# Performance work log

Measured on AMD Instinct MI355X. Metric: run time of the kernel, lower is better.

The kernel has to match this reference:

```python
import jax, jax.numpy as jnp
import numpy as np
import math

H = 1024
B, S = 4, 2048

def setup_inputs() -> dict:
    key = jax.random.key(0)
    k0, k1, k2, k3, k4 = jax.random.split(key, 5)
    scale = 1.0 / math.sqrt(H)
    return {
        "input_seq_rep": jax.random.normal(k0, (B, S, H), dtype=jnp.float32),
        "Wk": jax.random.uniform(k1, (H, H), dtype=jnp.float32, minval=-scale, maxval=scale),
        "bk": jax.random.uniform(k2, (H,), dtype=jnp.float32, minval=-scale, maxval=scale),
        "Wq": jax.random.uniform(k3, (H, H), dtype=jnp.float32, minval=-scale, maxval=scale),
        "bq": jax.random.uniform(k4, (H,), dtype=jnp.float32, minval=-scale, maxval=scale),
        "k_mul": 64,
    }

def reference(input_seq_rep, Wk, bk, Wq, bq, k_mul):
    b, s, h = input_seq_rep.shape
    x = jax.nn.relu(input_seq_rep)
    # torch Linear: x @ W.T + b
    k = jnp.einsum('bsh,oh->bso', x, Wk) + bk   # key (also used as value)
    q = jnp.einsum('bsh,oh->bso', x, Wq) + bq
    scores = jnp.einsum('bqh,bkh->bqk', q, k) / jnp.sqrt(jnp.float32(h))
    # Faithful mask: banded window only for batch index 0; other batches all-zero mask
    i = jnp.arange(s)[:, None]
    j = jnp.arange(s)[None, :]
    band = ((j <= i) & (j >= i - k_mul)).astype(jnp.float32)  # (S,S)
    mask = jnp.zeros((b, s, s), dtype=jnp.float32).at[0].set(band)
    scores = jnp.where(mask == 0, jnp.float32(-1e9), scores)
    p_attn = jax.nn.softmax(scores, axis=-1)
    out = jnp.einsum('bqk,bkh->bqh', p_attn, k)
    return out, p_attn
```

## Files before the change

kernel.cpp:

```cpp
#include <hip/hip_runtime.h>

#define SD 2048
#define HD 1024
#define BD 4

typedef __bf16 bf16_t;
typedef bf16_t bf16x8 __attribute__((ext_vector_type(8)));
typedef float f32x4 __attribute__((ext_vector_type(4)));
typedef unsigned short ushortx8 __attribute__((ext_vector_type(8)));
typedef unsigned short ushort_t;

__device__ inline unsigned short f2bf(float f) {
  return __builtin_bit_cast(unsigned short, (__bf16)f);
}

__device__ inline float bf2f(unsigned short u) {
  return __builtin_bit_cast(float, (unsigned)u << 16);
}

__device__ inline void gload_lds16(const void* g, void* l) {
  __builtin_amdgcn_global_load_lds(
      (const __attribute__((address_space(1))) void*)g,
      (__attribute__((address_space(3))) void*)l, 16, 0, 0);
}

template <int ROWS>
__device__ inline void stage_rows(const ushort_t* __restrict__ src, int r0, int k0,
                                  int tid, ushort_t* lds)
{
#pragma unroll
  for (int it = 0; it < ROWS / 32; ++it) {
    int c   = it * 256 + tid;
    int row = c >> 3;
    int kc8 = c & 7;
    int kcs = kc8 ^ (row & 7);
    gload_lds16(&src[(size_t)(r0 + row) * HD + k0 + kcs * 8], &lds[c * 8]);
  }
}

__device__ inline bf16x8 lds_frag(const ushort_t* l, int row, int kc8) {
  int kcs = kc8 ^ (row & 7);
  return *(const bf16x8*)&l[row * 64 + kcs * 8];
}

__global__ __launch_bounds__(256) void prep(
    const float* __restrict__ X, const float* __restrict__ Wk,
    const float* __restrict__ Wq, ushort_t* __restrict__ Xb,
    ushort_t* __restrict__ Wkb, ushort_t* __restrict__ Wqb)
{
  const int n8x = SD * HD / 8;
  const int n8w = HD * HD / 8;
  const int e = blockIdx.x * 256 + threadIdx.x;
  const float4* s4; ushortx8* d8; int idx; bool relu;
  if (e < n8x)            { s4 = (const float4*)X;  d8 = (ushortx8*)Xb;  idx = e;             relu = true; }
  else if (e < n8x + n8w) { s4 = (const float4*)Wk; d8 = (ushortx8*)Wkb; idx = e - n8x;       relu = false; }
  else                    { s4 = (const float4*)Wq; d8 = (ushortx8*)Wqb; idx = e - n8x - n8w; relu = false; }
  float4 a = s4[idx * 2], b4 = s4[idx * 2 + 1];
  float v[8] = {a.x, a.y, a.z, a.w, b4.x, b4.y, b4.z, b4.w};
  ushortx8 o;
#pragma unroll
  for (int j = 0; j < 8; ++j) {
    float f = v[j];
    if (relu) f = fmaxf(f, 0.0f);
    o[j] = f2bf(f);
  }
  d8[idx] = o;
}

__global__ __launch_bounds__(256, 2) void gemm_kq(
    const ushort_t* __restrict__ Xb, const ushort_t* __restrict__ Wkb,
    const ushort_t* __restrict__ Wqb, const float* __restrict__ bk,
    const float* __restrict__ bq, ushort_t* __restrict__ Kb,
    ushort_t* __restrict__ Qb, const float* __restrict__ X,
    float* __restrict__ part, float* __restrict__ patRest)
{
  __shared__ __align__(16) ushort_t lA[2][8192];
  __shared__ __align__(16) ushort_t lB[2][8192];

  const int bid = blockIdx.x;
  const int tid = threadIdx.x;

  if (bid >= 352) {
    const int f = bid - 352;
    const int nf4 = 3 * SD * (SD / 4);
    const float uf = 1.0f / SD;
    float4 v = make_float4(uf, uf, uf, uf);
    float4* p4 = (float4*)patRest;
    for (int e = f * 256 + tid; e < nf4; e += 384 * 256) p4[e] = v;
    return;
  }
  if (bid >= 256) {
    const int cid = bid - 256;
    const int b = cid >> 5;
    const int sub = cid & 31;
    const float4* Xp = (const float4*)(X + (size_t)(b + 1) * SD * HD + (size_t)sub * 64 * HD);
    float4 acc = make_float4(0.f, 0.f, 0.f, 0.f);
#pragma unroll 4
    for (int rr = 0; rr < 64; ++rr) {
      float4 v = Xp[rr * 256 + tid];
      acc.x += fmaxf(v.x, 0.f); acc.y += fmaxf(v.y, 0.f);
      acc.z += fmaxf(v.z, 0.f); acc.w += fmaxf(v.w, 0.f);
    }
    ((float4*)part)[((size_t)b * 32 + sub) * 256 + tid] = acc;
    return;
  }

  const int wg = ((bid & 7) << 5) | (bid >> 3);
  const int bm = wg >> 4, bn = wg & 15;
  const int half = bn >> 3;
  const ushort_t* Bm = half ? Wqb : Wkb;
  const int m0 = bm * 128, n0 = (bn & 7) * 128;

  const int lane = tid & 63;
  const int wave = tid >> 6;
  const int wm = wave >> 1, wn = wave & 1;

  f32x4 acc[4][4] = {};

  stage_rows<128>(Xb, m0, 0, tid, lA[0]);
  stage_rows<128>(Bm, n0, 0, tid, lB[0]);
  __syncthreads();

  for (int t = 0; t < 16; ++t) {
    const int cur = t & 1;
    if (t < 15) {
      stage_rows<128>(Xb, m0, (t + 1) * 64, tid, lA[cur ^ 1]);
      stage_rows<128>(Bm, n0, (t + 1) * 64, tid, lB[cur ^ 1]);
    }
#pragma unroll
    for (int h = 0; h < 2; ++h) {
      bf16x8 af[4], bfr[4];
#pragma unroll
      for (int mi = 0; mi < 4; ++mi)
        af[mi] = lds_frag(lA[cur], wm * 64 + mi * 16 + (lane & 15), h * 4 + (lane >> 4));
#pragma unroll
      for (int ni = 0; ni < 4; ++ni)
        bfr[ni] = lds_frag(lB[cur], wn * 64 + ni * 16 + (lane & 15), h * 4 + (lane >> 4));
#pragma unroll
      for (int mi = 0; mi < 4; ++mi)
#pragma unroll
        for (int ni = 0; ni < 4; ++ni)
          acc[mi][ni] = __builtin_amdgcn_mfma_f32_16x16x32_bf16(af[mi], bfr[ni], acc[mi][ni], 0, 0, 0);
    }
    __syncthreads();
  }

  const int rb = (lane >> 4) * 4;
  const int cc = lane & 15;
  const float* bias = half ? bq : bk;
  ushort_t* dst = half ? Qb : Kb;
#pragma unroll
  for (int ni = 0; ni < 4; ++ni) {
    int col = n0 + wn * 64 + ni * 16 + cc;
    float bv = bias[col];
#pragma unroll
    for (int mi = 0; mi < 4; ++mi) {
#pragma unroll
      for (int j = 0; j < 4; ++j) {
        int row = m0 + wm * 64 + mi * 16 + rb + j;
        dst[(size_t)row * HD + col] = f2bf(acc[mi][ni][j] + bv);
      }
    }
  }
}

__global__ __launch_bounds__(256, 2) void band_cm(
    const ushort_t* __restrict__ Q, const ushort_t* __restrict__ K,
    float* __restrict__ Sb0, float* __restrict__ Sb1,
    const float* __restrict__ part, const float* __restrict__ Wk,
    const float* __restrict__ bk, float* __restrict__ cm)
{
  __shared__ __align__(16) char smem[32768];
  const int bid = blockIdx.x;
  const int tid = threadIdx.x;

  if (bid < 126) {
    const int tt = bid >> 1;
    const int ks = bid & 1;
    const int blk = (tt + 1) >> 1;
    const int tcol = (tt + 1) & 1;
    const int m0 = blk * 64;
    const int n0 = (blk - 1 + tcol) * 64;
    float* Sb = ks ? Sb1 : Sb0;

    const int lane = tid & 63;
    const int wave = tid >> 6;
    const int wm = wave >> 1, wn = wave & 1;

    ushort_t* lA = (ushort_t*)smem;
    ushort_t* lB = (ushort_t*)(smem + 16384);

    f32x4 acc[2][2] = {};

    const int kbase = ks * 512;
    stage_rows<64>(Q, m0, kbase, tid, lA);
    stage_rows<64>(K, n0, kbase, tid, lB);
    __syncthreads();

    for (int t = 0; t < 8; ++t) {
      const int cur = t & 1;
      if (t < 7) {
        stage_rows<64>(Q, m0, kbase + (t + 1) * 64, tid, lA + (cur ^ 1) * 4096);
        stage_rows<64>(K, n0, kbase + (t + 1) * 64, tid, lB + (cur ^ 1) * 4096);
      }
#pragma unroll
      for (int h = 0; h < 2; ++h) {
        bf16x8 af[2], bfr[2];
#pragma unroll
        for (int mi = 0; mi < 2; ++mi)
          af[mi] = lds_frag(lA + cur * 4096, wm * 32 + mi * 16 + (lane & 15), h * 4 + (lane >> 4));
#pragma unroll
        for (int ni = 0; ni < 2; ++ni)
          bfr[ni] = lds_frag(lB + cur * 4096, wn * 32 + ni * 16 + (lane & 15), h * 4 + (lane >> 4));
#pragma unroll
        for (int mi = 0; mi < 2; ++mi)
#pragma unroll
          for (int ni = 0; ni < 2; ++ni)
            acc[mi][ni] = __builtin_amdgcn_mfma_f32_16x16x32_bf16(af[mi], bfr[ni], acc[mi][ni], 0, 0, 0);
      }
      __syncthreads();
    }

    const int rb = (lane >> 4) * 4;
    const int cc = lane & 15;
#pragma unroll
    for (int ni = 0; ni < 2; ++ni) {
      int ccol = tcol * 64 + wn * 32 + ni * 16 + cc;
#pragma unroll
      for (int mi = 0; mi < 2; ++mi)
#pragma unroll
        for (int j = 0; j < 4; ++j) {
          int row = m0 + wm * 32 + mi * 16 + rb + j;
          Sb[(size_t)row * 128 + ccol] = acc[mi][ni][j] * 0.03125f;
        }
    }
    return;
  }

  {
    const int cid = bid - 126;
    const int b = cid >> 4, og = cid & 15;
    float* xs = (float*)smem;
#pragma unroll
    for (int k = 0; k < 4; ++k) {
      int h = tid + 256 * k;
      float a = 0;
#pragma unroll 8
      for (int rc = 0; rc < 32; ++rc) a += part[((size_t)b * 32 + rc) * HD + h];
      xs[h] = a;
    }
    __syncthreads();
    const int o = og * 64 + (tid >> 2);
    const int q = tid & 3;
    const f32x4* wr = (const f32x4*)(Wk + (size_t)o * HD);
    const f32x4* x4 = (const f32x4*)xs;
    float a = 0;
#pragma unroll 8
    for (int i = 0; i < 64; ++i) {
      f32x4 w = wr[q * 64 + i], x = x4[q * 64 + i];
      a += w[0] * x[0] + w[1] * x[1] + w[2] * x[2] + w[3] * x[3];
    }
    a += __shfl_xor(a, 1);
    a += __shfl_xor(a, 2);
    if (q == 0) cm[b * HD + o] = a * (1.0f / SD) + bk[o];
  }
}

__global__ __launch_bounds__(256, 2) void pv_epi(
    const float* __restrict__ Sb0, const float* __restrict__ Sb1,
    const ushort_t* __restrict__ Kb, const float* __restrict__ cm,
    float* __restrict__ out0, float* __restrict__ P0,
    float* __restrict__ out123)
{
  __shared__ __align__(16) float smem[15488];
  const int bid = blockIdx.x;
  const int t = threadIdx.x;

  if (bid < 512) {
    float* Ks  = smem;
    float* spl = smem + 12288;
    const int i0 = (bid >> 3) * 32;
    const int hc = bid & 7;

    for (int e = t; e < 96 * 16; e += 256) {
      int lr = e >> 4, c8 = e & 15;
      int gr = i0 - 64 + lr;
      if (gr < 0) gr = 0;
      ushortx8 u = *(const ushortx8*)&Kb[(size_t)gr * HD + hc * 128 + c8 * 8];
      f32x4 f0 = {bf2f(u[0]), bf2f(u[1]), bf2f(u[2]), bf2f(u[3])};
      f32x4 f1 = {bf2f(u[4]), bf2f(u[5]), bf2f(u[6]), bf2f(u[7])};
      *(f32x4*)&Ks[lr * 128 + c8 * 8]     = f0;
      *(f32x4*)&Ks[lr * 128 + c8 * 8 + 4] = f1;
    }

    {
      const int r = t >> 3, sub = t & 7;
      const int i = i0 + r;
      const int jlo = (i >= 64) ? i - 64 : 0;
      const int scoff = i0 & 32;
      float sv[12];
      float m = -1e30f;
#pragma unroll
      for (int k = 0; k < 12; ++k) {
        int lj = sub + 8 * k;
        int gj = i0 - 64 + lj;
        bool val = (gj >= jlo) && (gj <= i);
        float s = -1e30f;
        if (val) {
          size_t sidx = (size_t)i * 128 + lj + scoff;
          s = Sb0[sidx] + Sb1[sidx];
        }
        sv[k] = s;
        m = fmaxf(m, s);
      }
#pragma unroll
      for (int off = 1; off < 8; off <<= 1) m = fmaxf(m, __shfl_xor(m, off));
      float p[12], sum = 0;
#pragma unroll
      for (int k = 0; k < 12; ++k) {
        p[k] = (sv[k] > -1e29f) ? __expf(sv[k] - m) : 0.0f;
        sum += p[k];
      }
#pragma unroll
      for (int off = 1; off < 8; off <<= 1) sum += __shfl_xor(sum, off);
      float inv = 1.0f / sum;
#pragma unroll
      for (int k = 0; k < 12; ++k) spl[r * 100 + sub + 8 * k] = p[k] * inv;
    }
    __syncthreads();

    const int r = t >> 3;
    const int g = t & 7;
    f32x4 a0 = {0,0,0,0}, a1 = {0,0,0,0}, a2 = {0,0,0,0}, a3 = {0,0,0,0};
    for (int lj = 0; lj < 96; ++lj) {
      float pv = spl[r * 100 + lj];
      const float* kr = &Ks[lj * 128 + g * 4];
      a0 += pv * *(const f32x4*)(kr);
      a1 += pv * *(const f32x4*)(kr + 32);
      a2 += pv * *(const f32x4*)(kr + 64);
      a3 += pv * *(const f32x4*)(kr + 96);
    }
    float* ob = out0 + (size_t)(i0 + r) * HD + hc * 128 + g * 4;
    *(f32x4*)(ob)      = a0;
    *(f32x4*)(ob + 32) = a1;
    *(f32x4*)(ob + 64) = a2;
    *(f32x4*)(ob + 96) = a3;
    return;
  }

  if (bid < 1024) {
    float* probs = smem;
    const int widx = t >> 6;
    const int lane = t & 63;
    const int i = (bid - 512) * 4 + widx;
    const int jlo = (i >= 64) ? i - 64 : 0;
    const int cnt = i - jlo + 1;
    const int base = ((i >> 6) - 1) * 64;

    float s0 = -1e30f;
    if (lane < cnt) {
      size_t c = (size_t)i * 128 + (jlo - base + lane);
      s0 = Sb0[c] + Sb1[c];
    }
    float s1 = -1e30f;
    if (cnt == 65) {
      size_t c = (size_t)i * 128 + (jlo - base + 64);
      s1 = Sb0[c] + Sb1[c];
    }
    float m = s0;
#pragma unroll
    for (int off = 1; off < 64; off <<= 1) m = fmaxf(m, __shfl_xor(m, off));
    m = fmaxf(m, s1);
    float p0 = (lane < cnt) ? __expf(s0 - m) : 0.0f;
    float p1 = (cnt == 65) ? __expf(s1 - m) : 0.0f;
    float sum = p0;
#pragma unroll
    for (int off = 1; off < 64; off <<= 1) sum += __shfl_xor(sum, off);
    sum += p1;
    float inv = 1.0f / sum;
    if (lane < cnt) probs[widx * 68 + lane] = p0 * inv;
    if (lane == 0 && cnt == 65) probs[widx * 68 + 64] = p1 * inv;
    __syncthreads();

    float4* rowp = (float4*)(P0 + (size_t)i * SD);
#pragma unroll
    for (int k = 0; k < 8; ++k) {
      int f4i = k * 64 + lane;
      int j0 = f4i * 4;
      float4 v = make_float4(0.f, 0.f, 0.f, 0.f);
      if (j0 + 3 >= jlo && j0 <= i) {
        float* vv = (float*)&v;
#pragma unroll
        for (int q = 0; q < 4; ++q) {
          int j = j0 + q;
          if (j >= jlo && j <= i) vv[q] = probs[widx * 68 + (j - jlo)];
        }
      }
      rowp[f4i] = v;
    }
    return;
  }

  {
    const int nf4 = 3 * SD * (HD / 4);
    const int per_b = SD * (HD / 4);
    const f32x4* cm4 = (const f32x4*)cm;
    f32x4* o4 = (f32x4*)out123;
    for (int idx = (bid - 1024) * 256 + t; idx < nf4; idx += 512 * 256) {
      int b = idx / per_b;
      int h4 = idx & (HD / 4 - 1);
      o4[idx] = cm4[b * (HD / 4) + h4];
    }
  }
}

extern "C" void kernel_launch(void* const* d_in, const int* in_sizes, int n_in,
                              void* d_out, int out_size, void* d_ws, size_t ws_size,
                              hipStream_t stream)
{
  (void)in_sizes; (void)n_in; (void)out_size; (void)ws_size;
  const float* X  = (const float*)d_in[0];
  const float* Wk = (const float*)d_in[1];
  const float* bk = (const float*)d_in[2];
  const float* Wq = (const float*)d_in[3];
  const float* bq = (const float*)d_in[4];

  float* out = (float*)d_out;
  float* pat = out + (size_t)BD * SD * HD;

  char* w = (char*)d_ws;
  ushort_t* Xb   = (ushort_t*)w; w += (size_t)SD * HD * 2;
  ushort_t* Wkb  = (ushort_t*)w; w += (size_t)HD * HD * 2;
  ushort_t* Wqb  = (ushort_t*)w; w += (size_t)HD * HD * 2;
  ushort_t* Kb0  = (ushort_t*)w; w += (size_t)SD * HD * 2;
  ushort_t* Q0b  = (ushort_t*)w; w += (size_t)SD * HD * 2;
  float*    part = (float*)w;    w += (size_t)3 * 32 * HD * 4;
  float*    cm   = (float*)w;    w += (size_t)3 * HD * 4;
  float*    Sb0  = (float*)w;    w += (size_t)SD * 128 * 4;
  float*    Sb1  = (float*)w;    w += (size_t)SD * 128 * 4;

  prep<<<2048, 256, 0, stream>>>(X, Wk, Wq, Xb, Wkb, Wqb);
  gemm_kq<<<736, 256, 0, stream>>>(Xb, Wkb, Wqb, bk, bq, Kb0, Q0b, X, part,
                                   pat + (size_t)SD * SD);
  band_cm<<<174, 256, 0, stream>>>(Q0b, Kb0, Sb0, Sb1, part, Wk, bk, cm);
  pv_epi<<<1536, 256, 0, stream>>>(Sb0, Sb1, Kb0, cm, out, pat, out + (size_t)SD * HD);
}
```

Baseline: 69.94 us.

## Fuse fp32-to-bf16 conversion into GEMM staging and move broadcast into band_cm

Removes the separate prep kernel: the projection GEMM now loads fp32 X and weights into registers, applies ReLU, converts them to bf16 and writes them swizzled into LDS, with the loads for the next tile issued ahead of the MFMA work. The broadcast of the per-batch column means into outputs for batches 1-3 moves from pv_epi into band_cm, which drops the cm buffer and 512 blocks from pv_epi. This removes one launch and the bf16 round trip through global memory. In exchange the GEMM reads twice the bytes per tile, holds more registers, and loses the async global-to-LDS path. band_cm's 48 mean blocks now also write the large broadcast region.

After: 75.76 us. 1.08x slower.

```diff
diff --git a/kernel.cpp b/kernel.cpp
--- a/kernel.cpp
+++ b/kernel.cpp
@@ -43,36 +43,47 @@
   return *(const bf16x8*)&l[row * 64 + kcs * 8];
 }
 
-__global__ __launch_bounds__(256) void prep(
+__device__ inline void stage_load(const float* __restrict__ src, int r0, int k0,
+                                  int tid, f32x4* regs)
+{
+#pragma unroll
+  for (int it = 0; it < 4; ++it) {
+    int c   = it * 256 + tid;
+    int row = c >> 3;
+    int kc8 = c & 7;
+    const float* g = &src[(size_t)(r0 + row) * HD + k0 + kc8 * 8];
+    regs[it * 2]     = *(const f32x4*)g;
+    regs[it * 2 + 1] = *(const f32x4*)(g + 4);
+  }
+}
+
+template <bool RELU>
+__device__ inline void stage_write(const f32x4* regs, int tid, ushort_t* lds)
+{
+#pragma unroll
+  for (int it = 0; it < 4; ++it) {
+    int c   = it * 256 + tid;
+    int row = c >> 3;
+    int kc8 = c & 7;
+    int kcs = kc8 ^ (row & 7);
+    f32x4 v0 = regs[it * 2], v1 = regs[it * 2 + 1];
+    ushortx8 o;
+#pragma unroll
+    for (int j = 0; j < 4; ++j) {
+      float f0 = v0[j], f1 = v1[j];
+      if (RELU) { f0 = fmaxf(f0, 0.f); f1 = fmaxf(f1, 0.f); }
+      o[j] = f2bf(f0); o[4 + j] = f2bf(f1);
+    }
+    *(ushortx8*)&lds[row * 64 + kcs * 8] = o;
+  }
+}
+
+__global__ __launch_bounds__(256, 2) void gemm_kq(
     const float* __restrict__ X, const float* __restrict__ Wk,
-    const float* __restrict__ Wq, ushort_t* __restrict__ Xb,
-    ushort_t* __restrict__ Wkb, ushort_t* __restrict__ Wqb)
-{
-  const int n8x = SD * HD / 8;
-  const int n8w = HD * HD / 8;
-  const int e = blockIdx.x * 256 + threadIdx.x;
-  const float4* s4; ushortx8* d8; int idx; bool relu;
-  if (e < n8x)            { s4 = (const float4*)X;  d8 = (ushortx8*)Xb;  idx = e;             relu = true; }
-  else if (e < n8x + n8w) { s4 = (const float4*)Wk; d8 = (ushortx8*)Wkb; idx = e - n8x;       relu = false; }
-  else                    { s4 = (const float4*)Wq; d8 = (ushortx8*)Wqb; idx = e - n8x - n8w; relu = false; }
-  float4 a = s4[idx * 2], b4 = s4[idx * 2 + 1];
-  float v[8] = {a.x, a.y, a.z, a.w, b4.x, b4.y, b4.z, b4.w};
-  ushortx8 o;
-#pragma unroll
-  for (int j = 0; j < 8; ++j) {
-    float f = v[j];
-    if (relu) f = fmaxf(f, 0.0f);
-    o[j] = f2bf(f);
-  }
-  d8[idx] = o;
-}
-
-__global__ __launch_bounds__(256, 2) void gemm_kq(
-    const ushort_t* __restrict__ Xb, const ushort_t* __restrict__ Wkb,
-    const ushort_t* __restrict__ Wqb, const float* __restrict__ bk,
+    const float* __restrict__ Wq, const float* __restrict__ bk,
     const float* __restrict__ bq, ushort_t* __restrict__ Kb,
-    ushort_t* __restrict__ Qb, const float* __restrict__ X,
-    float* __restrict__ part, float* __restrict__ patRest)
+    ushort_t* __restrict__ Qb, float* __restrict__ part,
+    float* __restrict__ patRest)
 {
   __shared__ __align__(16) ushort_t lA[2][8192];
   __shared__ __align__(16) ushort_t lB[2][8192];
@@ -108,7 +119,7 @@
   const int wg = ((bid & 7) << 5) | (bid >> 3);
   const int bm = wg >> 4, bn = wg & 15;
   const int half = bn >> 3;
-  const ushort_t* Bm = half ? Wqb : Wkb;
+  const float* Bsrc = half ? Wq : Wk;
   const int m0 = bm * 128, n0 = (bn & 7) * 128;
 
   const int lane = tid & 63;
@@ -116,16 +127,19 @@
   const int wm = wave >> 1, wn = wave & 1;
 
   f32x4 acc[4][4] = {};
-
-  stage_rows<128>(Xb, m0, 0, tid, lA[0]);
-  stage_rows<128>(Bm, n0, 0, tid, lB[0]);
+  f32x4 ra[8], rb[8];
+
+  stage_load(X, m0, 0, tid, ra);
+  stage_load(Bsrc, n0, 0, tid, rb);
+  stage_write<true>(ra, tid, lA[0]);
+  stage_write<false>(rb, tid, lB[0]);
   __syncthreads();
 
   for (int t = 0; t < 16; ++t) {
     const int cur = t & 1;
     if (t < 15) {
-      stage_rows<128>(Xb, m0, (t + 1) * 64, tid, lA[cur ^ 1]);
-      stage_rows<128>(Bm, n0, (t + 1) * 64, tid, lB[cur ^ 1]);
+      stage_load(X, m0, (t + 1) * 64, tid, ra);
+      stage_load(Bsrc, n0, (t + 1) * 64, tid, rb);
     }
 #pragma unroll
     for (int h = 0; h < 2; ++h) {
@@ -142,10 +156,14 @@
         for (int ni = 0; ni < 4; ++ni)
           acc[mi][ni] = __builtin_amdgcn_mfma_f32_16x16x32_bf16(af[mi], bfr[ni], acc[mi][ni], 0, 0, 0);
     }
-    __syncthreads();
-  }
-
-  const int rb = (lane >> 4) * 4;
+    if (t < 15) {
+      stage_write<true>(ra, tid, lA[cur ^ 1]);
+      stage_write<false>(rb, tid, lB[cur ^ 1]);
+    }
+    __syncthreads();
+  }
+
+  const int rb2 = (lane >> 4) * 4;
   const int cc = lane & 15;
   const float* bias = half ? bq : bk;
   ushort_t* dst = half ? Qb : Kb;
@@ -157,7 +175,7 @@
     for (int mi = 0; mi < 4; ++mi) {
 #pragma unroll
       for (int j = 0; j < 4; ++j) {
-        int row = m0 + wm * 64 + mi * 16 + rb + j;
+        int row = m0 + wm * 64 + mi * 16 + rb2 + j;
         dst[(size_t)row * HD + col] = f2bf(acc[mi][ni][j] + bv);
       }
     }
@@ -168,7 +186,7 @@
     const ushort_t* __restrict__ Q, const ushort_t* __restrict__ K,
     float* __restrict__ Sb0, float* __restrict__ Sb1,
     const float* __restrict__ part, const float* __restrict__ Wk,
-    const float* __restrict__ bk, float* __restrict__ cm)
+    const float* __restrict__ bk, float* __restrict__ out123)
 {
   __shared__ __align__(16) char smem[32768];
   const int bid = blockIdx.x;
@@ -241,6 +259,7 @@
     const int cid = bid - 126;
     const int b = cid >> 4, og = cid & 15;
     float* xs = (float*)smem;
+    float* res = xs + HD;
 #pragma unroll
     for (int k = 0; k < 4; ++k) {
       int h = tid + 256 * k;
@@ -262,15 +281,25 @@
     }
     a += __shfl_xor(a, 1);
     a += __shfl_xor(a, 2);
-    if (q == 0) cm[b * HD + o] = a * (1.0f / SD) + bk[o];
+    if (q == 0) res[tid >> 2] = a * (1.0f / SD) + bk[o];
+    __syncthreads();
+
+    const int rpt = tid >> 4;
+    const int cq  = tid & 15;
+    f32x4 val = *(const f32x4*)&res[cq * 4];
+    float* base = out123 + (size_t)b * SD * HD + og * 64 + cq * 4;
+#pragma unroll 4
+    for (int pass = 0; pass < 128; ++pass) {
+      int s = pass * 16 + rpt;
+      *(f32x4*)&base[(size_t)s * HD] = val;
+    }
   }
 }
 
 __global__ __launch_bounds__(256, 2) void pv_epi(
     const float* __restrict__ Sb0, const float* __restrict__ Sb1,
-    const ushort_t* __restrict__ Kb, const float* __restrict__ cm,
-    float* __restrict__ out0, float* __restrict__ P0,
-    float* __restrict__ out123)
+    const ushort_t* __restrict__ Kb, float* __restrict__ out0,
+    float* __restrict__ P0)
 {
   __shared__ __align__(16) float smem[15488];
   const int bid = blockIdx.x;
@@ -348,7 +377,7 @@
     return;
   }
 
-  if (bid < 1024) {
+  {
     float* probs = smem;
     const int widx = t >> 6;
     const int lane = t & 63;
@@ -398,19 +427,6 @@
       }
       rowp[f4i] = v;
     }
-    return;
-  }
-
-  {
-    const int nf4 = 3 * SD * (HD / 4);
-    const int per_b = SD * (HD / 4);
-    const f32x4* cm4 = (const f32x4*)cm;
-    f32x4* o4 = (f32x4*)out123;
-    for (int idx = (bid - 1024) * 256 + t; idx < nf4; idx += 512 * 256) {
-      int b = idx / per_b;
-      int h4 = idx & (HD / 4 - 1);
-      o4[idx] = cm4[b * (HD / 4) + h4];
-    }
   }
 }
 
@@ -429,19 +445,15 @@
   float* pat = out + (size_t)BD * SD * HD;
 
   char* w = (char*)d_ws;
-  ushort_t* Xb   = (ushort_t*)w; w += (size_t)SD * HD * 2;
-  ushort_t* Wkb  = (ushort_t*)w; w += (size_t)HD * HD * 2;
-  ushort_t* Wqb  = (ushort_t*)w; w += (size_t)HD * HD * 2;
   ushort_t* Kb0  = (ushort_t*)w; w += (size_t)SD * HD * 2;
   ushort_t* Q0b  = (ushort_t*)w; w += (size_t)SD * HD * 2;
   float*    part = (float*)w;    w += (size_t)3 * 32 * HD * 4;
-  float*    cm   = (float*)w;    w += (size_t)3 * HD * 4;
   float*    Sb0  = (float*)w;    w += (size_t)SD * 128 * 4;
   float*    Sb1  = (float*)w;    w += (size_t)SD * 128 * 4;
 
-  prep<<<2048, 256, 0, stream>>>(X, Wk, Wq, Xb, Wkb, Wqb);
-  gemm_kq<<<736, 256, 0, stream>>>(Xb, Wkb, Wqb, bk, bq, Kb0, Q0b, X, part,
+  gemm_kq<<<736, 256, 0, stream>>>(X, Wk, Wq, bk, bq, Kb0, Q0b, part,
                                    pat + (size_t)SD * SD);
-  band_cm<<<174, 256, 0, stream>>>(Q0b, Kb0, Sb0, Sb1, part, Wk, bk, cm);
-  pv_epi<<<1536, 256, 0, stream>>>(Sb0, Sb1, Kb0, cm, out, pat, out + (size_t)SD * HD);
-}
+  band_cm<<<174, 256, 0, stream>>>(Q0b, Kb0, Sb0, Sb1, part, Wk, bk,
+                                   out + (size_t)SD * HD);
+  pv_epi<<<1024, 256, 0, stream>>>(Sb0, Sb1, Kb0, out, pat);
+}
```

## Fuse batch-0 probability row writes into PV blocks; zero-fill in GEMM kernel

Applied to the files above, without the earlier changes.

Removes the separate block range in pv_epi that recomputed the banded softmax and wrote full batch-0 probability rows. The zero background of batch-0 p_attn is now written by the idle tail blocks of gemm_kq alongside the uniform fill, and the PV blocks with hc==0 scatter the in-band probabilities they already computed. This drops a redundant softmax pass and 512 blocks of launch. The catch is that the in-band writes are now ordered against the zero-fill only through the kernel boundary, and the scattered writes are small and uncoalesced.

Measured after the change: 73.26 us. 4.8% more time.

```diff
diff --git a/kernel.cpp b/kernel.cpp
--- a/kernel.cpp
+++ b/kernel.cpp
@@ -72,7 +72,7 @@
     const ushort_t* __restrict__ Wqb, const float* __restrict__ bk,
     const float* __restrict__ bq, ushort_t* __restrict__ Kb,
     ushort_t* __restrict__ Qb, const float* __restrict__ X,
-    float* __restrict__ part, float* __restrict__ patRest)
+    float* __restrict__ part, float* __restrict__ pat)
 {
   __shared__ __align__(16) ushort_t lA[2][8192];
   __shared__ __align__(16) ushort_t lB[2][8192];
@@ -82,11 +82,13 @@
 
   if (bid >= 352) {
     const int f = bid - 352;
-    const int nf4 = 3 * SD * (SD / 4);
+    const int nf4 = SD * (SD / 4);
     const float uf = 1.0f / SD;
-    float4 v = make_float4(uf, uf, uf, uf);
-    float4* p4 = (float4*)patRest;
-    for (int e = f * 256 + tid; e < nf4; e += 384 * 256) p4[e] = v;
+    float4 z = make_float4(0.f, 0.f, 0.f, 0.f);
+    float4 u = make_float4(uf, uf, uf, uf);
+    float4* p4 = (float4*)pat;
+    for (int e = f * 256 + tid; e < 4 * nf4; e += 384 * 256)
+      p4[e] = (e < nf4) ? z : u;
     return;
   }
   if (bid >= 256) {
@@ -325,7 +327,13 @@
       for (int off = 1; off < 8; off <<= 1) sum += __shfl_xor(sum, off);
       float inv = 1.0f / sum;
 #pragma unroll
-      for (int k = 0; k < 12; ++k) spl[r * 100 + sub + 8 * k] = p[k] * inv;
+      for (int k = 0; k < 12; ++k) {
+        int lj = sub + 8 * k;
+        float pv = p[k] * inv;
+        spl[r * 100 + lj] = pv;
+        if (hc == 0 && sv[k] > -1e29f)
+          P0[(size_t)i * SD + (i0 - 64 + lj)] = pv;
+      }
     }
     __syncthreads();
 
@@ -348,65 +356,12 @@
     return;
   }
 
-  if (bid < 1024) {
-    float* probs = smem;
-    const int widx = t >> 6;
-    const int lane = t & 63;
-    const int i = (bid - 512) * 4 + widx;
-    const int jlo = (i >= 64) ? i - 64 : 0;
-    const int cnt = i - jlo + 1;
-    const int base = ((i >> 6) - 1) * 64;
-
-    float s0 = -1e30f;
-    if (lane < cnt) {
-      size_t c = (size_t)i * 128 + (jlo - base + lane);
-      s0 = Sb0[c] + Sb1[c];
-    }
-    float s1 = -1e30f;
-    if (cnt == 65) {
-      size_t c = (size_t)i * 128 + (jlo - base + 64);
-      s1 = Sb0[c] + Sb1[c];
-    }
-    float m = s0;
-#pragma unroll
-    for (int off = 1; off < 64; off <<= 1) m = fmaxf(m, __shfl_xor(m, off));
-    m = fmaxf(m, s1);
-    float p0 = (lane < cnt) ? __expf(s0 - m) : 0.0f;
-    float p1 = (cnt == 65) ? __expf(s1 - m) : 0.0f;
-    float sum = p0;
-#pragma unroll
-    for (int off = 1; off < 64; off <<= 1) sum += __shfl_xor(sum, off);
-    sum += p1;
-    float inv = 1.0f / sum;
-    if (lane < cnt) probs[widx * 68 + lane] = p0 * inv;
-    if (lane == 0 && cnt == 65) probs[widx * 68 + 64] = p1 * inv;
-    __syncthreads();
-
-    float4* rowp = (float4*)(P0 + (size_t)i * SD);
-#pragma unroll
-    for (int k = 0; k < 8; ++k) {
-      int f4i = k * 64 + lane;
-      int j0 = f4i * 4;
-      float4 v = make_float4(0.f, 0.f, 0.f, 0.f);
-      if (j0 + 3 >= jlo && j0 <= i) {
-        float* vv = (float*)&v;
-#pragma unroll
-        for (int q = 0; q < 4; ++q) {
-          int j = j0 + q;
-          if (j >= jlo && j <= i) vv[q] = probs[widx * 68 + (j - jlo)];
-        }
-      }
-      rowp[f4i] = v;
-    }
-    return;
-  }
-
   {
     const int nf4 = 3 * SD * (HD / 4);
     const int per_b = SD * (HD / 4);
     const f32x4* cm4 = (const f32x4*)cm;
     f32x4* o4 = (f32x4*)out123;
-    for (int idx = (bid - 1024) * 256 + t; idx < nf4; idx += 512 * 256) {
+    for (int idx = (bid - 512) * 256 + t; idx < nf4; idx += 512 * 256) {
       int b = idx / per_b;
       int h4 = idx & (HD / 4 - 1);
       o4[idx] = cm4[b * (HD / 4) + h4];
@@ -440,8 +395,7 @@
   float*    Sb1  = (float*)w;    w += (size_t)SD * 128 * 4;
 
   prep<<<2048, 256, 0, stream>>>(X, Wk, Wq, Xb, Wkb, Wqb);
-  gemm_kq<<<736, 256, 0, stream>>>(Xb, Wkb, Wqb, bk, bq, Kb0, Q0b, X, part,
-                                   pat + (size_t)SD * SD);
+  gemm_kq<<<736, 256, 0, stream>>>(Xb, Wkb, Wqb, bk, bq, Kb0, Q0b, X, part, pat);
   band_cm<<<174, 256, 0, stream>>>(Q0b, Kb0, Sb0, Sb1, part, Wk, bk, cm);
-  pv_epi<<<1536, 256, 0, stream>>>(Sb0, Sb1, Kb0, cm, out, pat, out + (size_t)SD * HD);
-}
+  pv_epi<<<1024, 256, 0, stream>>>(Sb0, Sb1, Kb0, cm, out, pat, out + (size_t)SD * HD);
+}
```
